# Performance work log

Hardware: AMD Instinct MI355X
Metric: run time of the kernel (lower is better)

Reference implementation:

```python
import math
import jax, jax.numpy as jnp
import numpy as np

POOLED_H, POOLED_W = 7, 7
SPATIAL_SCALE = 0.25
SAMPLING_RATIO = 2  # grid points per bin per axis (fixed > 0 -> static shapes)


def setup_inputs() -> dict:
    key = jax.random.key(0)
    ks = jax.random.split(key, 7)
    B, C, H, W = 2, 256, 200, 176
    N = 1024
    x = jax.random.normal(ks[0], (B, C, H, W), dtype=jnp.float32)
    batch = jax.random.randint(ks[1], (N,), 0, B).astype(jnp.float32)
    cw = jax.random.uniform(ks[2], (N,), minval=0.0, maxval=W / SPATIAL_SCALE)
    ch = jax.random.uniform(ks[3], (N,), minval=0.0, maxval=H / SPATIAL_SCALE)
    rw = jax.random.uniform(ks[4], (N,), minval=16.0, maxval=256.0)
    rh = jax.random.uniform(ks[5], (N,), minval=16.0, maxval=256.0)
    theta = jax.random.uniform(ks[6], (N,), minval=-math.pi, maxval=math.pi)
    z = jnp.zeros((N,), jnp.float32)
    # rois0 layout (per module forward): col0=batch_ind, col1=center_h, col2=center_w,
    # col4=roi_height, col5=roi_width, col7=yaw (rad); cols 3,6 unused here.
    rois0 = jnp.stack([batch, ch, cw, z, rh, rw, z, theta], axis=1)
    return {"input": x, "rois0": rois0}


def _roi_align_rotated(feat, rois):
    # feat: [B, C, H, W]; rois: [N, 6] = [batch, cw, ch, rw, rh, theta_deg]
    B, C, H, W = feat.shape
    N = rois.shape[0]
    GH = GW = SAMPLING_RATIO

    b = rois[:, 0].astype(jnp.int32)
    cw = rois[:, 1] * SPATIAL_SCALE - 0.5
    ch = rois[:, 2] * SPATIAL_SCALE - 0.5
    rw = rois[:, 3] * SPATIAL_SCALE
    rh = rois[:, 4] * SPATIAL_SCALE
    theta = rois[:, 5] * (math.pi / 180.0)

    bin_h = rh / POOLED_H   # [N]
    bin_w = rw / POOLED_W
    start_h = -rh * 0.5
    start_w = -rw * 0.5

    def col(v):  # [N] -> [N,1,1,1,1]
        return v[:, None, None, None, None]

    ph = jnp.arange(POOLED_H, dtype=feat.dtype)[None, :, None, None, None]
    pw = jnp.arange(POOLED_W, dtype=feat.dtype)[None, None, :, None, None]
    iy = jnp.arange(GH, dtype=feat.dtype)[None, None, None, :, None]
    ix = jnp.arange(GW, dtype=feat.dtype)[None, None, None, None, :]

    # local (un-rotated) sample coords inside the ROI
    yy = col(start_h) + ph * col(bin_h) + (iy + 0.5) * col(bin_h) / GH  # [N,PH,1,GH,1]
    xx = col(start_w) + pw * col(bin_w) + (ix + 0.5) * col(bin_w) / GW  # [N,1,PW,1,GW]

    cosT, sinT = col(jnp.cos(theta)), col(jnp.sin(theta))
    y = yy * cosT - xx * sinT + col(ch)  # [N,PH,PW,GH,GW]
    x = yy * sinT + xx * cosT + col(cw)
    y = jnp.broadcast_to(y, (N, POOLED_H, POOLED_W, GH, GW))
    x = jnp.broadcast_to(x, (N, POOLED_H, POOLED_W, GH, GW))

    # bilinear interpolation (detectron2 semantics)
    valid = (y >= -1.0) & (y <= H) & (x >= -1.0) & (x <= W)
    yc = jnp.clip(y, 0.0, None)
    xc = jnp.clip(x, 0.0, None)
    y0 = jnp.floor(yc).astype(jnp.int32)
    x0 = jnp.floor(xc).astype(jnp.int32)
    yc = jnp.where(y0 >= H - 1, jnp.asarray(H - 1, feat.dtype), yc)
    xc = jnp.where(x0 >= W - 1, jnp.asarray(W - 1, feat.dtype), xc)
    y0 = jnp.minimum(y0, H - 1)
    x0 = jnp.minimum(x0, W - 1)
    y1 = jnp.minimum(y0 + 1, H - 1)
    x1 = jnp.minimum(x0 + 1, W - 1)

    ly = yc - y0.astype(feat.dtype)
    lx = xc - x0.astype(feat.dtype)
    hy, hx = 1.0 - ly, 1.0 - lx

    bb = b[:, None, None, None, None]  # broadcast with [N,PH,PW,GH,GW]

    def gather(yi, xi):
        # -> [N,PH,PW,GH,GW,C]
        return feat[bb, :, yi, xi]

    w1 = (hy * hx)[..., None]
    w2 = (hy * lx)[..., None]
    w3 = (ly * hx)[..., None]
    w4 = (ly * lx)[..., None]
    v = (w1 * gather(y0, x0) + w2 * gather(y0, x1)
         + w3 * gather(y1, x0) + w4 * gather(y1, x1))
    v = v * valid[..., None].astype(feat.dtype)

    out = v.mean(axis=(3, 4))          # average over sampling grid -> [N,PH,PW,C]
    return out.transpose(0, 3, 1, 2)    # [N,C,PH,PW]


def reference(input, rois0):
    # module forward: permute roi columns, rad -> deg (kernel converts back)
    rois = rois0[:, jnp.array([0, 2, 1, 5, 4, 7])]
    rois = rois.at[:, -1].multiply(180.0 / math.pi)
    return _roi_align_rotated(input, rois)
```

## Files before the change

### kernel.cpp

```cpp
#include <hip/hip_runtime.h>
#include <hip/hip_fp16.h>

#define B_  2
#define C_  256
#define H_  200
#define W_  176
constexpr int HW_ = H_ * W_;
constexpr float SCALE_ = 0.25f;

__global__ __launch_bounds__(256) void nchw_to_nhwc_h(const float* __restrict__ in,
                                                      __half* __restrict__ out,
                                                      const float* __restrict__ rois,
                                                      int N, int* __restrict__ perm) {
    __shared__ float tile[32][65];
    __shared__ int   fill[8];
    __shared__ int   spill[1024];
    __shared__ int   spill_cnt;

    const int b   = blockIdx.z;
    const int hw0 = blockIdx.x * 32;
    const int c0  = blockIdx.y * 64;
    const int tx  = threadIdx.x;
    const int ty  = threadIdx.y;

    const float* src = in + (size_t)b * C_ * HW_;
    __half*      dst = out + (size_t)b * HW_ * C_;

#pragma unroll
    for (int jj = 0; jj < 8; ++jj) {
        const int j = ty + jj * 8;
        tile[tx][j] = src[(size_t)(c0 + j) * HW_ + hw0 + tx];
    }
    __syncthreads();

    const int tid  = ty * 32 + tx;
    const int k    = tid & 31;
    const int row0 = tid >> 5;
#pragma unroll
    for (int rr = 0; rr < 4; ++rr) {
        const int i = row0 + rr * 8;
        __half2 hv;
        hv.x = __float2half(tile[i][2 * k]);
        hv.y = __float2half(tile[i][2 * k + 1]);
        __half2* orow = (__half2*)(dst + (size_t)(hw0 + i) * C_ + c0);
        orow[k] = hv;
    }

    if (blockIdx.x == 0 && blockIdx.y == 0 && blockIdx.z == 0) {
        if (tid < 8) fill[tid] = 0;
        if (tid == 0) spill_cnt = 0;
        __syncthreads();
        if (N > 1024 || (N & 7) != 0) {
            for (int i = tid; i < N; i += 256) perm[i] = i;
            return;
        }
        const int S = N >> 3;
        for (int i = tid; i < N; i += 256) {
            const float* r = rois + (size_t)i * 8;
            const int   rb = (int)r[0];
            const float cy = r[1] * SCALE_;
            const float cx = r[2] * SCALE_;
            const int bk = rb * 4 + (cy >= (float)H_ * 0.5f ? 2 : 0)
                                  + (cx >= (float)W_ * 0.5f ? 1 : 0);
            const int rank = atomicAdd(&fill[bk], 1);
            if (rank < S) perm[bk + 8 * rank] = i;
            else          spill[atomicAdd(&spill_cnt, 1)] = i;
        }
        __syncthreads();
        if (tid == 0) {
            int idx = 0;
            for (int g = 0; g < 8; ++g) {
                const int have = fill[g] < S ? fill[g] : S;
                for (int r = have; r < S; ++r) perm[g + 8 * r] = spill[idx++];
            }
        }
    }
}

template <bool TR>
__global__ __launch_bounds__(256, 8) void roi_gather(const void* __restrict__ featv,
                                                     const float* __restrict__ rois,
                                                     const int* __restrict__ perm,
                                                     float* __restrict__ out) {
    __shared__ int2   s_geo[49 * 16];
    __shared__ __half s_tile[128 * 49];
    __shared__ int    s_bbase;

    const int n     = TR ? perm[blockIdx.x] : blockIdx.x;
    const int chalf = blockIdx.y;
    const int tid   = threadIdx.x;

    if (tid < 196) {
        const float* r = rois + (size_t)n * 8;
        const int   b   = (int)r[0];
        const float chv = r[1] * SCALE_ - 0.5f;
        const float cwv = r[2] * SCALE_ - 0.5f;
        const float rhv = r[4] * SCALE_;
        const float rwv = r[5] * SCALE_;
        const float deg = r[7] * 57.29577951308232f;
        const float th  = deg * 0.017453292519943295f;
        if (tid == 0) s_bbase = b * C_ * HW_;

        const float bin_h = rhv / 7.0f;
        const float bin_w = rwv / 7.0f;

        const int sp  = tid;
        const int bin = sp >> 2;
        const int s   = sp & 3;
        const int iy  = s >> 1, ix = s & 1;
        const int ph  = bin / 7, pw = bin % 7;

        float yy = -rhv * 0.5f + (float)ph * bin_h + (((float)iy + 0.5f) * bin_h) * 0.5f;
        float xx = -rwv * 0.5f + (float)pw * bin_w + (((float)ix + 0.5f) * bin_w) * 0.5f;

        const float ct = cosf(th), st = sinf(th);
        const float y = yy * ct - xx * st + chv;
        const float x = yy * st + xx * ct + cwv;

        const bool valid = (y >= -1.0f) && (y <= (float)H_) &&
                           (x >= -1.0f) && (x <= (float)W_);
        float yc = fmaxf(y, 0.0f);
        float xc = fmaxf(x, 0.0f);
        int   y0 = (int)floorf(yc);
        int   x0 = (int)floorf(xc);
        if (y0 >= H_ - 1) yc = (float)(H_ - 1);
        if (x0 >= W_ - 1) xc = (float)(W_ - 1);
        y0 = min(y0, H_ - 1);
        x0 = min(x0, W_ - 1);
        const int y1 = min(y0 + 1, H_ - 1);
        const int x1 = min(x0 + 1, W_ - 1);

        const float ly = yc - (float)y0;
        const float lx = xc - (float)x0;
        const float hy = 1.0f - ly, hx = 1.0f - lx;
        const float sc = valid ? 0.25f : 0.0f;

        const int base = TR ? (b * H_) : 0;
        const int o00 = ((base + y0) * W_ + x0) * (TR ? 512 : 1);
        const int o01 = ((base + y0) * W_ + x1) * (TR ? 512 : 1);
        const int o10 = ((base + y1) * W_ + x0) * (TR ? 512 : 1);
        const int o11 = ((base + y1) * W_ + x1) * (TR ? 512 : 1);

        const float w0 = hy * hx * sc, w1 = hy * lx * sc;
        const float w2 = ly * hx * sc, w3 = ly * lx * sc;

        const int e = sp * 4;
        if (TR) {
            __half2 p0 = __half2half2(__float2half(w0));
            __half2 p1 = __half2half2(__float2half(w1));
            __half2 p2 = __half2half2(__float2half(w2));
            __half2 p3 = __half2half2(__float2half(w3));
            s_geo[e + 0] = make_int2(o00, *(int*)&p0);
            s_geo[e + 1] = make_int2(o01, *(int*)&p1);
            s_geo[e + 2] = make_int2(o10, *(int*)&p2);
            s_geo[e + 3] = make_int2(o11, *(int*)&p3);
        } else {
            s_geo[e + 0] = make_int2(o00, __float_as_int(w0));
            s_geo[e + 1] = make_int2(o01, __float_as_int(w1));
            s_geo[e + 2] = make_int2(o10, __float_as_int(w2));
            s_geo[e + 3] = make_int2(o11, __float_as_int(w3));
        }
    }
    __syncthreads();

    const int cq = tid & 63;
    const int wv = tid >> 6;
    const int bbase = s_bbase;

    const char*  fb   = (const char*)featv;
    const float* ff   = (const float*)featv;
    const unsigned loff = (unsigned)(chalf * 64 + cq) * 4u;
    const int    c    = chalf * 128 + 2 * cq;

    for (int bin = wv; bin < 49; bin += 4) {
        const int e = bin * 16;
        if (TR) {
            __half2 acc = __half2half2(__float2half(0.0f));
#pragma unroll
            for (int j = 0; j < 16; ++j) {
                const int2 g = s_geo[e + j];
                const __half2 hv = *(const __half2*)(fb + ((unsigned)g.x + loff));
                const __half2 w2 = *(const __half2*)&g.y;
                acc = __hfma2(w2, hv, acc);
            }
            s_tile[(2 * cq) * 49 + bin]     = __low2half(acc);
            s_tile[(2 * cq + 1) * 49 + bin] = __high2half(acc);
        } else {
            float accx = 0.0f, accy = 0.0f;
#pragma unroll
            for (int j = 0; j < 16; ++j) {
                const int2  g = s_geo[e + j];
                const float w = __int_as_float(g.y);
                accx += w * ff[(size_t)(bbase + c * HW_ + g.x)];
                accy += w * ff[(size_t)(bbase + (c + 1) * HW_ + g.x)];
            }
            s_tile[(2 * cq) * 49 + bin]     = __float2half(accx);
            s_tile[(2 * cq + 1) * 49 + bin] = __float2half(accy);
        }
    }
    __syncthreads();

    float* ob = out + (size_t)n * (C_ * 49) + (size_t)chalf * (128 * 49);
    for (int i = tid; i < 128 * 49; i += 256) {
        __builtin_nontemporal_store(__half2float(s_tile[i]), &ob[i]);
    }
}

extern "C" void kernel_launch(void* const* d_in, const int* in_sizes, int n_in,
                              void* d_out, int out_size, void* d_ws, size_t ws_size,
                              hipStream_t stream) {
    const float* x    = (const float*)d_in[0];
    const float* rois = (const float*)d_in[1];
    float*       out  = (float*)d_out;
    const int N = in_sizes[1] / 8;

    const size_t tr_bytes = (size_t)B_ * HW_ * C_ * sizeof(__half);
    const size_t perm_bytes = (size_t)N * sizeof(int);
    if (ws_size >= tr_bytes + perm_bytes && N <= 1024) {
        __half* xt   = (__half*)d_ws;
        int*    perm = (int*)((char*)d_ws + tr_bytes);
        dim3 tb(32, 8);
        dim3 tg(HW_ / 32, C_ / 64, B_);
        nchw_to_nhwc_h<<<tg, tb, 0, stream>>>(x, xt, rois, N, perm);
        dim3 gg(N, 2);
        roi_gather<true><<<gg, 256, 0, stream>>>(xt, rois, perm, out);
    } else {
        dim3 gg(N, 2);
        roi_gather<false><<<gg, 256, 0, stream>>>(x, rois, nullptr, out);
    }
}
```

Before: 47.67 us.

## Process all channels per ROI in one 512-thread block with wider loads

The transposed-path gather kernel now handles all 256 channels of an ROI in a single 512-thread block instead of splitting channels across two blocks. Each lane loads 8 bytes (two half2) per sample, and two independent accumulator pairs are kept per lane. This halves the per-ROI geometry setup (trig, bilinear weights) and gives more memory-level parallelism. The costs are a strided shared-memory read during the output write, a division by 49 per output element, and fewer resident blocks per CU. The fallback path is split into its own non-template kernel with plain stores.

```diff
diff --git a/kernel.cpp b/kernel.cpp
--- a/kernel.cpp
+++ b/kernel.cpp
@@ -77,18 +77,15 @@
     }
 }
 
-template <bool TR>
-__global__ __launch_bounds__(256, 8) void roi_gather(const void* __restrict__ featv,
-                                                     const float* __restrict__ rois,
-                                                     const int* __restrict__ perm,
-                                                     float* __restrict__ out) {
+__global__ __launch_bounds__(512, 8) void roi_gather_tr(const void* __restrict__ featv,
+                                                        const float* __restrict__ rois,
+                                                        const int* __restrict__ perm,
+                                                        float* __restrict__ out) {
     __shared__ int2   s_geo[49 * 16];
-    __shared__ __half s_tile[128 * 49];
-    __shared__ int    s_bbase;
-
-    const int n     = TR ? perm[blockIdx.x] : blockIdx.x;
-    const int chalf = blockIdx.y;
-    const int tid   = threadIdx.x;
+    __shared__ __half2 s_tile[128 * 49];
+
+    const int n   = perm[blockIdx.x];
+    const int tid = threadIdx.x;
 
     if (tid < 196) {
         const float* r = rois + (size_t)n * 8;
@@ -99,7 +96,6 @@
         const float rwv = r[5] * SCALE_;
         const float deg = r[7] * 57.29577951308232f;
         const float th  = deg * 0.017453292519943295f;
-        if (tid == 0) s_bbase = b * C_ * HW_;
 
         const float bin_h = rhv / 7.0f;
         const float bin_w = rwv / 7.0f;
@@ -135,75 +131,143 @@
         const float hy = 1.0f - ly, hx = 1.0f - lx;
         const float sc = valid ? 0.25f : 0.0f;
 
-        const int base = TR ? (b * H_) : 0;
-        const int o00 = ((base + y0) * W_ + x0) * (TR ? 512 : 1);
-        const int o01 = ((base + y0) * W_ + x1) * (TR ? 512 : 1);
-        const int o10 = ((base + y1) * W_ + x0) * (TR ? 512 : 1);
-        const int o11 = ((base + y1) * W_ + x1) * (TR ? 512 : 1);
-
-        const float w0 = hy * hx * sc, w1 = hy * lx * sc;
-        const float w2 = ly * hx * sc, w3 = ly * lx * sc;
-
+        const int o00 = ((b * H_ + y0) * W_ + x0) * 512;
+        const int o01 = ((b * H_ + y0) * W_ + x1) * 512;
+        const int o10 = ((b * H_ + y1) * W_ + x0) * 512;
+        const int o11 = ((b * H_ + y1) * W_ + x1) * 512;
+
+        __half2 p0 = __half2half2(__float2half(hy * hx * sc));
+        __half2 p1 = __half2half2(__float2half(hy * lx * sc));
+        __half2 p2 = __half2half2(__float2half(ly * hx * sc));
+        __half2 p3 = __half2half2(__float2half(ly * lx * sc));
         const int e = sp * 4;
-        if (TR) {
-            __half2 p0 = __half2half2(__float2half(w0));
-            __half2 p1 = __half2half2(__float2half(w1));
-            __half2 p2 = __half2half2(__float2half(w2));
-            __half2 p3 = __half2half2(__float2half(w3));
-            s_geo[e + 0] = make_int2(o00, *(int*)&p0);
-            s_geo[e + 1] = make_int2(o01, *(int*)&p1);
-            s_geo[e + 2] = make_int2(o10, *(int*)&p2);
-            s_geo[e + 3] = make_int2(o11, *(int*)&p3);
-        } else {
-            s_geo[e + 0] = make_int2(o00, __float_as_int(w0));
-            s_geo[e + 1] = make_int2(o01, __float_as_int(w1));
-            s_geo[e + 2] = make_int2(o10, __float_as_int(w2));
-            s_geo[e + 3] = make_int2(o11, __float_as_int(w3));
-        }
+        s_geo[e + 0] = make_int2(o00, *(int*)&p0);
+        s_geo[e + 1] = make_int2(o01, *(int*)&p1);
+        s_geo[e + 2] = make_int2(o10, *(int*)&p2);
+        s_geo[e + 3] = make_int2(o11, *(int*)&p3);
+    }
+    __syncthreads();
+
+    const int lane = tid & 63;
+    const int wv   = tid >> 6;
+    const char* fb = (const char*)featv;
+    const unsigned loff = (unsigned)lane * 8u;
+
+    for (int bin = wv; bin < 49; bin += 8) {
+        const int e = bin * 16;
+        __half2 ax0 = __half2half2(__float2half(0.0f));
+        __half2 ay0 = ax0, ax1 = ax0, ay1 = ax0;
+#pragma unroll
+        for (int j = 0; j < 16; j += 2) {
+            const int2 g0 = s_geo[e + j];
+            const int2 g1 = s_geo[e + j + 1];
+            const int2 v0 = *(const int2*)(fb + ((unsigned)g0.x + loff));
+            const int2 v1 = *(const int2*)(fb + ((unsigned)g1.x + loff));
+            const __half2 w0 = *(const __half2*)&g0.y;
+            const __half2 w1 = *(const __half2*)&g1.y;
+            ax0 = __hfma2(w0, *(const __half2*)&v0.x, ax0);
+            ay0 = __hfma2(w0, *(const __half2*)&v0.y, ay0);
+            ax1 = __hfma2(w1, *(const __half2*)&v1.x, ax1);
+            ay1 = __hfma2(w1, *(const __half2*)&v1.y, ay1);
+        }
+        ax0 = __hadd2(ax0, ax1);
+        ay0 = __hadd2(ay0, ay1);
+        s_tile[(2 * lane) * 49 + bin]     = ax0;
+        s_tile[(2 * lane + 1) * 49 + bin] = ay0;
+    }
+    __syncthreads();
+
+    const __half* th_ = (const __half*)s_tile;
+    float* ob = out + (size_t)n * (C_ * 49);
+    for (int i = tid; i < 256 * 49; i += 512) {
+        const int c = i / 49, bn = i - c * 49;
+        const float v = __half2float(th_[(c >> 1) * 98 + 2 * bn + (c & 1)]);
+        __builtin_nontemporal_store(v, &ob[i]);
+    }
+}
+
+__global__ __launch_bounds__(256, 8) void roi_gather_fb(const float* __restrict__ ff,
+                                                        const float* __restrict__ rois,
+                                                        float* __restrict__ out) {
+    __shared__ int2   s_geo[49 * 16];
+    __shared__ __half s_tile[128 * 49];
+    __shared__ int    s_bbase;
+
+    const int n     = blockIdx.x;
+    const int chalf = blockIdx.y;
+    const int tid   = threadIdx.x;
+
+    if (tid < 196) {
+        const float* r = rois + (size_t)n * 8;
+        const int   b   = (int)r[0];
+        const float chv = r[1] * SCALE_ - 0.5f;
+        const float cwv = r[2] * SCALE_ - 0.5f;
+        const float rhv = r[4] * SCALE_;
+        const float rwv = r[5] * SCALE_;
+        const float deg = r[7] * 57.29577951308232f;
+        const float th  = deg * 0.017453292519943295f;
+        if (tid == 0) s_bbase = b * C_ * HW_;
+
+        const float bin_h = rhv / 7.0f;
+        const float bin_w = rwv / 7.0f;
+        const int sp  = tid;
+        const int bin = sp >> 2;
+        const int s   = sp & 3;
+        const int iy  = s >> 1, ix = s & 1;
+        const int ph  = bin / 7, pw = bin % 7;
+
+        float yy = -rhv * 0.5f + (float)ph * bin_h + (((float)iy + 0.5f) * bin_h) * 0.5f;
+        float xx = -rwv * 0.5f + (float)pw * bin_w + (((float)ix + 0.5f) * bin_w) * 0.5f;
+        const float ct = cosf(th), st = sinf(th);
+        const float y = yy * ct - xx * st + chv;
+        const float x = yy * st + xx * ct + cwv;
+        const bool valid = (y >= -1.0f) && (y <= (float)H_) &&
+                           (x >= -1.0f) && (x <= (float)W_);
+        float yc = fmaxf(y, 0.0f);
+        float xc = fmaxf(x, 0.0f);
+        int   y0 = (int)floorf(yc);
+        int   x0 = (int)floorf(xc);
+        if (y0 >= H_ - 1) yc = (float)(H_ - 1);
+        if (x0 >= W_ - 1) xc = (float)(W_ - 1);
+        y0 = min(y0, H_ - 1);
+        x0 = min(x0, W_ - 1);
+        const int y1 = min(y0 + 1, H_ - 1);
+        const int x1 = min(x0 + 1, W_ - 1);
+        const float ly = yc - (float)y0;
+        const float lx = xc - (float)x0;
+        const float hy = 1.0f - ly, hx = 1.0f - lx;
+        const float sc = valid ? 0.25f : 0.0f;
+
+        const int e = sp * 4;
+        s_geo[e + 0] = make_int2((y0 * W_ + x0), __float_as_int(hy * hx * sc));
+        s_geo[e + 1] = make_int2((y0 * W_ + x1), __float_as_int(hy * lx * sc));
+        s_geo[e + 2] = make_int2((y1 * W_ + x0), __float_as_int(ly * hx * sc));
+        s_geo[e + 3] = make_int2((y1 * W_ + x1), __float_as_int(ly * lx * sc));
     }
     __syncthreads();
 
     const int cq = tid & 63;
     const int wv = tid >> 6;
     const int bbase = s_bbase;
-
-    const char*  fb   = (const char*)featv;
-    const float* ff   = (const float*)featv;
-    const unsigned loff = (unsigned)(chalf * 64 + cq) * 4u;
-    const int    c    = chalf * 128 + 2 * cq;
+    const int c  = chalf * 128 + 2 * cq;
 
     for (int bin = wv; bin < 49; bin += 4) {
+        float accx = 0.0f, accy = 0.0f;
         const int e = bin * 16;
-        if (TR) {
-            __half2 acc = __half2half2(__float2half(0.0f));
-#pragma unroll
-            for (int j = 0; j < 16; ++j) {
-                const int2 g = s_geo[e + j];
-                const __half2 hv = *(const __half2*)(fb + ((unsigned)g.x + loff));
-                const __half2 w2 = *(const __half2*)&g.y;
-                acc = __hfma2(w2, hv, acc);
-            }
-            s_tile[(2 * cq) * 49 + bin]     = __low2half(acc);
-            s_tile[(2 * cq + 1) * 49 + bin] = __high2half(acc);
-        } else {
-            float accx = 0.0f, accy = 0.0f;
-#pragma unroll
-            for (int j = 0; j < 16; ++j) {
-                const int2  g = s_geo[e + j];
-                const float w = __int_as_float(g.y);
-                accx += w * ff[(size_t)(bbase + c * HW_ + g.x)];
-                accy += w * ff[(size_t)(bbase + (c + 1) * HW_ + g.x)];
-            }
-            s_tile[(2 * cq) * 49 + bin]     = __float2half(accx);
-            s_tile[(2 * cq + 1) * 49 + bin] = __float2half(accy);
-        }
+#pragma unroll
+        for (int j = 0; j < 16; ++j) {
+            const int2  g = s_geo[e + j];
+            const float w = __int_as_float(g.y);
+            accx += w * ff[(size_t)(bbase + c * HW_ + g.x)];
+            accy += w * ff[(size_t)(bbase + (c + 1) * HW_ + g.x)];
+        }
+        s_tile[(2 * cq) * 49 + bin]     = __float2half(accx);
+        s_tile[(2 * cq + 1) * 49 + bin] = __float2half(accy);
     }
     __syncthreads();
 
     float* ob = out + (size_t)n * (C_ * 49) + (size_t)chalf * (128 * 49);
-    for (int i = tid; i < 128 * 49; i += 256) {
-        __builtin_nontemporal_store(__half2float(s_tile[i]), &ob[i]);
-    }
+    for (int i = tid; i < 128 * 49; i += 256) ob[i] = __half2float(s_tile[i]);
 }
 
 extern "C" void kernel_launch(void* const* d_in, const int* in_sizes, int n_in,
@@ -222,10 +286,9 @@
         dim3 tb(32, 8);
         dim3 tg(HW_ / 32, C_ / 64, B_);
         nchw_to_nhwc_h<<<tg, tb, 0, stream>>>(x, xt, rois, N, perm);
-        dim3 gg(N, 2);
-        roi_gather<true><<<gg, 256, 0, stream>>>(xt, rois, perm, out);
+        roi_gather_tr<<<N, 512, 0, stream>>>(xt, rois, perm, out);
     } else {
         dim3 gg(N, 2);
-        roi_gather<false><<<gg, 256, 0, stream>>>(x, rois, nullptr, out);
-    }
-}
+        roi_gather_fb<<<gg, 256, 0, stream>>>(x, rois, out);
+    }
+}
```

After: 53.30 us. 1.12x slower.
